# Kernel optimization log

Measured on AMD Instinct MI355X. Metric: run time of the kernel, lower is better.

The kernel has to match this reference:

```python
import jax, jax.numpy as jnp
import numpy as np

N, B, C, H = 1024, 4, 1024, 8
D = C // H  # head dim = 128


def setup_inputs() -> dict:
    key = jax.random.key(0)
    ks = jax.random.split(key, 10)
    f = lambda k, s: jax.random.normal(k, s, dtype=jnp.float32)
    w = lambda k: f(k, (C, C)) * 0.02  # torch Linear weight layout (out, in)
    return {
        "query_reg": f(ks[0], (N, B, C)),
        "key_reg": f(ks[1], (N, B, C)),
        "query_cls": f(ks[2], (N, B, C)),
        "key_cls": f(ks[3], (N, B, C)),
        "value": f(ks[4], (N, B, C)),
        "W_q_reg": w(ks[5]),
        "W_k_reg": w(ks[6]),
        "W_q_cls": w(ks[7]),
        "W_k_cls": w(ks[8]),
        "W_v": w(ks[9]),
    }


def _proj_heads(x, W):
    # x: (N, B, C); torch Linear: y = x @ W.T -> reshape (N,B,H,D) -> (B,H,N,D)
    y = jnp.einsum('nbc,dc->nbd', x, W)
    return y.reshape(N, B, H, D).transpose(1, 2, 0, 3)


def _l2norm(x):
    return x / jnp.linalg.norm(x, axis=-1, keepdims=True)


def reference(query_reg, key_reg, query_cls, key_cls, value,
              W_q_reg, W_k_reg, W_q_cls, W_k_cls, W_v):
    q_reg = _l2norm(_proj_heads(query_reg, W_q_reg))  # (B,H,N,D)
    k_reg = _l2norm(_proj_heads(key_reg, W_k_reg))
    q_cls = _l2norm(_proj_heads(query_cls, W_q_cls))
    k_cls = _l2norm(_proj_heads(key_cls, W_k_cls))
    v = _proj_heads(value, W_v)

    attn_reg = jax.nn.softmax(jnp.einsum('bhnd,bhmd->bhnm', q_reg, k_reg), axis=-1)
    attn_cls = jax.nn.softmax(jnp.einsum('bhnd,bhmd->bhnm', q_cls, k_cls), axis=-1)
    attn = (attn_reg + attn_cls) * 0.5  # (B,H,N,N)

    x = jnp.einsum('bhnm,bhmd->bhnd', attn, v)  # (B,H,N,D)
    x = x.transpose(0, 2, 1, 3).reshape(B, N, C)  # (B,N,C)
    return (x.transpose(1, 0, 2), attn)  # ((N,B,C), (B,H,N,N))
```

## Files before the change

kernel.cpp:

```cpp
#include <hip/hip_runtime.h>

#define DEVINL __device__ __forceinline__

typedef unsigned short u16;
typedef float f32x4 __attribute__((ext_vector_type(4)));
typedef __bf16 bf16x8 __attribute__((ext_vector_type(8)));

constexpr int N_ = 1024, B_ = 4, C_ = 1024, H_ = 8, D_ = 128;
constexpr int NB = N_ * B_;
constexpr int BH = B_ * H_;

DEVINL u16 f2bf(float f) {
  unsigned u = __builtin_bit_cast(unsigned, f);
  u += 0x7fffu + ((u >> 16) & 1u);
  return (u16)(u >> 16);
}
DEVINL float bf2f(u16 v) { return __builtin_bit_cast(float, ((unsigned)v) << 16); }

typedef __attribute__((address_space(1))) void gv_t;
typedef __attribute__((address_space(3))) void lv_t;
DEVINL void gload16(const void* g, void* l) {
  __builtin_amdgcn_global_load_lds((gv_t*)(unsigned long long)g,
                                   (lv_t*)(unsigned)(unsigned long long)l, 16, 0, 0);
}
DEVINL bf16x8 ld_frag(const u16* p) { return *(const bf16x8*)p; }
DEVINL f32x4 mfma16(bf16x8 a, bf16x8 b, f32x4 c) {
  return __builtin_amdgcn_mfma_f32_16x16x32_bf16(a, b, c, 0, 0, 0);
}

struct ConvArgs { const float* s[10]; u16* d[10]; int n[10]; };

__global__ __launch_bounds__(256) void k_convert(ConvArgs a) {
  const int which = blockIdx.y;
  const int i = (blockIdx.x * 256 + threadIdx.x) * 8;
  if (i >= a.n[which]) return;
  const float* s = a.s[which] + i;
  float4 v0 = *(const float4*)s;
  float4 v1 = *(const float4*)(s + 4);
  union { uint4 v; u16 r[8]; } u;
  u.r[0] = f2bf(v0.x); u.r[1] = f2bf(v0.y); u.r[2] = f2bf(v0.z); u.r[3] = f2bf(v0.w);
  u.r[4] = f2bf(v1.x); u.r[5] = f2bf(v1.y); u.r[6] = f2bf(v1.z); u.r[7] = f2bf(v1.w);
  *(uint4*)(a.d[which] + i) = u.v;
}

struct ProjArgs { const u16* X[5]; const u16* W[5]; u16* O[5]; };

__global__ __launch_bounds__(256) void k_proj(ProjArgs a) {
  __shared__ u16 lA[128 * 64];
  __shared__ u16 lB[128 * 64];
  __shared__ float lred[128][2];
  const int tid = threadIdx.x, w = tid >> 6, lane = tid & 63;
  const int qd = lane >> 4, m16 = lane & 15;
  const int wr = w >> 1, wc = w & 1;
  const int r0 = blockIdx.y * 128, d0 = blockIdx.x * 128;
  const u16* __restrict__ X = a.X[blockIdx.z];
  const u16* __restrict__ W = a.W[blockIdx.z];
  u16* __restrict__ O = a.O[blockIdx.z];
  const bool donorm = blockIdx.z < 4;

  f32x4 acc[4][4];
  const f32x4 fz = {0.f, 0.f, 0.f, 0.f};
#pragma unroll
  for (int i = 0; i < 4; ++i)
#pragma unroll
    for (int j = 0; j < 4; ++j) acc[i][j] = fz;

  for (int k0 = 0; k0 < C_; k0 += 64) {
    __syncthreads();
#pragma unroll
    for (int i = 0; i < 4; ++i) {
      int p = i * 256 + tid, row = p >> 3, cp = p & 7, cl = cp ^ (row & 7);
      gload16(X + (size_t)(r0 + row) * C_ + k0 + cl * 8, &lA[p * 8]);
    }
#pragma unroll
    for (int i = 0; i < 4; ++i) {
      int p = i * 256 + tid, row = p >> 3, cp = p & 7, cl = cp ^ (row & 7);
      gload16(W + (size_t)(d0 + row) * C_ + k0 + cl * 8, &lB[p * 8]);
    }
    __syncthreads();
#pragma unroll
    for (int ks = 0; ks < 2; ++ks) {
      bf16x8 af[4], bfr[4];
#pragma unroll
      for (int t = 0; t < 4; ++t) {
        int row = wr * 64 + t * 16 + m16;
        af[t] = ld_frag(&lA[row * 64 + (((ks * 4 + qd) ^ (row & 7)) * 8)]);
        int col = wc * 64 + t * 16 + m16;
        bfr[t] = ld_frag(&lB[col * 64 + (((ks * 4 + qd) ^ (col & 7)) * 8)]);
      }
#pragma unroll
      for (int rt = 0; rt < 4; ++rt)
#pragma unroll
        for (int ct = 0; ct < 4; ++ct)
          acc[rt][ct] = mfma16(af[rt], bfr[ct], acc[rt][ct]);
    }
  }
  if (donorm) {
    float s[4][4];
#pragma unroll
    for (int rt = 0; rt < 4; ++rt)
#pragma unroll
      for (int rg = 0; rg < 4; ++rg) {
        float t = 0.f;
#pragma unroll
        for (int ct = 0; ct < 4; ++ct) t += acc[rt][ct][rg] * acc[rt][ct][rg];
        s[rt][rg] = t;
      }
#pragma unroll
    for (int off = 1; off < 16; off <<= 1)
#pragma unroll
      for (int rt = 0; rt < 4; ++rt)
#pragma unroll
        for (int rg = 0; rg < 4; ++rg) s[rt][rg] += __shfl_xor(s[rt][rg], off);
    if (m16 == 0) {
#pragma unroll
      for (int rt = 0; rt < 4; ++rt)
#pragma unroll
        for (int rg = 0; rg < 4; ++rg)
          lred[wr * 64 + rt * 16 + qd * 4 + rg][wc] = s[rt][rg];
    }
  }
  __syncthreads();
  float inv[4][4];
#pragma unroll
  for (int rt = 0; rt < 4; ++rt)
#pragma unroll
    for (int rg = 0; rg < 4; ++rg) {
      if (donorm) {
        int row = wr * 64 + rt * 16 + qd * 4 + rg;
        inv[rt][rg] = rsqrtf(lred[row][0] + lred[row][1]);
      } else inv[rt][rg] = 1.0f;
    }
#pragma unroll
  for (int rt = 0; rt < 4; ++rt)
#pragma unroll
    for (int ct = 0; ct < 4; ++ct)
#pragma unroll
      for (int rg = 0; rg < 4; ++rg) {
        int row = r0 + wr * 64 + rt * 16 + qd * 4 + rg;
        int col = d0 + wc * 64 + ct * 16 + m16;
        int n = row >> 2, b = row & 3, h = col >> 7, d = col & 127;
        O[(((size_t)(b * H_ + h)) * N_ + n) * D_ + d] = f2bf(acc[rt][ct][rg] * inv[rt][rg]);
      }
}

__global__ __launch_bounds__(256) void k_transpose(const u16* __restrict__ v,
                                                   u16* __restrict__ vt) {
  __shared__ u16 tile[128][65];
  const int bh = blockIdx.y, n0 = blockIdx.x * 64;
  const u16* src = v + (size_t)bh * N_ * D_;
  u16* dst = vt + (size_t)bh * D_ * N_;
  union U8 { uint4 v; u16 s[8]; };
#pragma unroll
  for (int it = 0; it < 4; ++it) {
    int c = it * 256 + threadIdx.x;
    int n = c >> 4, dc = (c & 15) * 8;
    U8 u; u.v = *(const uint4*)(src + (size_t)(n0 + n) * D_ + dc);
#pragma unroll
    for (int j = 0; j < 8; ++j) tile[dc + j][n] = u.s[j];
  }
  __syncthreads();
#pragma unroll
  for (int it = 0; it < 4; ++it) {
    int c = it * 256 + threadIdx.x;
    int d = c >> 3, nc = (c & 7) * 8;
    U8 u;
#pragma unroll
    for (int j = 0; j < 8; ++j) u.s[j] = tile[d][nc + j];
    *(uint4*)(dst + (size_t)d * N_ + n0 + nc) = u.v;
  }
}

__global__ __launch_bounds__(512, 2) void k_attn(const u16* __restrict__ qr,
                                                 const u16* __restrict__ kr,
                                                 const u16* __restrict__ qc,
                                                 const u16* __restrict__ kc,
                                                 const u16* __restrict__ vt,
                                                 float* __restrict__ out0,
                                                 float* __restrict__ out1) {
  __shared__ u16 lP[2][32 * 136];
  __shared__ float lred[2][8][32];
  const int flat = blockIdx.x + (blockIdx.y << 5);
  const int xcd = flat & 7, kk = flat >> 3;
  const int bh = (xcd << 2) + (kk >> 5);
  const int n0 = (kk & 31) * 32;
  const int b = bh >> 3, h = bh & 7;
  const size_t base = (size_t)bh * N_ * D_;
  const int tid = threadIdx.x, w = tid >> 6, lane = tid & 63;
  const int qd = lane >> 4, m16 = lane & 15;

  bf16x8 qf[2][2][4];
#pragma unroll
  for (int ct = 0; ct < 2; ++ct)
#pragma unroll
    for (int ks = 0; ks < 4; ++ks) {
      size_t ro = base + (size_t)(n0 + ct * 16 + m16) * D_ + ks * 32 + qd * 8;
      qf[0][ct][ks] = ld_frag(qr + ro);
      qf[1][ct][ks] = ld_frag(qc + ro);
    }

  const u16* krp = kr + base + (size_t)(w * 16 + m16) * D_;
  const u16* kcp = kc + base + (size_t)(w * 16 + m16) * D_;

  uint2 pst[2][8][2];
  float psum[2][2] = {{0.f, 0.f}, {0.f, 0.f}};
  const f32x4 fz = {0.f, 0.f, 0.f, 0.f};

#pragma unroll
  for (int mt = 0; mt < 8; ++mt) {
    const size_t moff = (size_t)mt * 128 * D_;
#pragma unroll
    for (int ty = 0; ty < 2; ++ty) {
      const u16* kp = (ty ? kcp : krp) + moff;
      bf16x8 af[4];
#pragma unroll
      for (int ks = 0; ks < 4; ++ks)
        af[ks] = ld_frag(kp + ks * 32 + qd * 8);
#pragma unroll
      for (int ct = 0; ct < 2; ++ct) {
        f32x4 acc = fz;
#pragma unroll
        for (int ks = 0; ks < 4; ++ks) acc = mfma16(af[ks], qf[ty][ct][ks], acc);
        union { uint2 u; u16 s[4]; } pk;
        float loc = 0.f;
#pragma unroll
        for (int rg = 0; rg < 4; ++rg) {
          float e = __expf(acc[rg]);
          loc += e;
          pk.s[rg] = f2bf(e);
        }
        psum[ty][ct] += loc;
        pst[ty][mt][ct] = pk.u;
      }
    }
  }

#pragma unroll
  for (int ty = 0; ty < 2; ++ty)
#pragma unroll
    for (int ct = 0; ct < 2; ++ct) {
      psum[ty][ct] += __shfl_xor(psum[ty][ct], 16);
      psum[ty][ct] += __shfl_xor(psum[ty][ct], 32);
    }
  if (qd == 0) {
#pragma unroll
    for (int ty = 0; ty < 2; ++ty)
#pragma unroll
      for (int ct = 0; ct < 2; ++ct) lred[ty][w][ct * 16 + m16] = psum[ty][ct];
  }
  __syncthreads();
  float il[2][2];
#pragma unroll
  for (int ty = 0; ty < 2; ++ty)
#pragma unroll
    for (int ct = 0; ct < 2; ++ct) {
      int n = ct * 16 + m16;
      float s = 0.f;
#pragma unroll
      for (int ww = 0; ww < 8; ++ww) s += lred[ty][ww][n];
      il[ty][ct] = 0.5f / s;
    }

  f32x4 xacc[2] = {fz, fz};
  float* attn = out1 + (size_t)bh * N_ * N_;
  const u16* vtb = vt + (size_t)bh * D_ * N_ + (size_t)(w * 16 + m16) * N_;

#pragma unroll
  for (int mt = 0; mt < 8; ++mt) {
    const int cur = mt & 1;
    const int m0 = mt * 128;
#pragma unroll
    for (int ct = 0; ct < 2; ++ct) {
      union { uint2 u; u16 s[4]; } ur, uc, pk;
      ur.u = pst[0][mt][ct];
      uc.u = pst[1][mt][ct];
      f32x4 pv;
#pragma unroll
      for (int rg = 0; rg < 4; ++rg) {
        pv[rg] = bf2f(ur.s[rg]) * il[0][ct] + bf2f(uc.s[rg]) * il[1][ct];
        pk.s[rg] = f2bf(pv[rg]);
      }
      const int nrow = n0 + ct * 16 + m16;
      const int mcol = m0 + w * 16 + qd * 4;
      *(f32x4*)(attn + (size_t)nrow * N_ + mcol) = pv;
      *(uint2*)&lP[cur][(ct * 16 + m16) * 136 + w * 16 + qd * 4] = pk.u;
    }
    __syncthreads();
#pragma unroll
    for (int ks = 0; ks < 4; ++ks) {
      bf16x8 pa[2];
#pragma unroll
      for (int ct = 0; ct < 2; ++ct)
        pa[ct] = ld_frag(&lP[cur][(ct * 16 + m16) * 136 + ks * 32 + qd * 8]);
      bf16x8 vb = ld_frag(vtb + m0 + ks * 32 + qd * 8);
#pragma unroll
      for (int ct = 0; ct < 2; ++ct)
        xacc[ct] = mfma16(pa[ct], vb, xacc[ct]);
    }
  }
#pragma unroll
  for (int ct = 0; ct < 2; ++ct)
#pragma unroll
    for (int rg = 0; rg < 4; ++rg) {
      int n = n0 + ct * 16 + qd * 4 + rg;
      int d = w * 16 + m16;
      out0[((size_t)n * B_ + b) * C_ + h * 128 + d] = xacc[ct][rg];
    }
}

extern "C" void kernel_launch(void* const* d_in, const int* in_sizes, int n_in,
                              void* d_out, int out_size, void* d_ws, size_t ws_size,
                              hipStream_t stream) {
  (void)in_sizes; (void)n_in; (void)out_size; (void)ws_size;
  const float* in_f[10];
  for (int i = 0; i < 10; ++i) in_f[i] = (const float*)d_in[i];

  u16* ws = (u16*)d_ws;
  u16* Xc[5], *Wc[5], *P[5];
  for (int i = 0; i < 5; ++i) Xc[i] = ws + (size_t)i * NB * C_;
  u16* wbase = ws + (size_t)5 * NB * C_;
  for (int i = 0; i < 5; ++i) Wc[i] = wbase + (size_t)i * C_ * C_;
  u16* pbase = wbase + (size_t)5 * C_ * C_;
  for (int i = 0; i < 5; ++i) P[i] = pbase + (size_t)i * BH * N_ * D_;
  u16* vt = pbase + (size_t)5 * BH * N_ * D_;

  float* out0 = (float*)d_out;
  float* out1 = out0 + (size_t)N_ * B_ * C_;

  ConvArgs ca;
  for (int i = 0; i < 5; ++i) { ca.s[i] = in_f[i];     ca.d[i] = Xc[i];  ca.n[i] = NB * C_; }
  for (int i = 0; i < 5; ++i) { ca.s[5+i] = in_f[5+i]; ca.d[5+i] = Wc[i]; ca.n[5+i] = C_ * C_; }
  k_convert<<<dim3(2048, 10), 256, 0, stream>>>(ca);

  ProjArgs pa;
  for (int i = 0; i < 5; ++i) { pa.X[i] = Xc[i]; pa.W[i] = Wc[i]; pa.O[i] = P[i]; }
  k_proj<<<dim3(C_ / 128, NB / 128, 5), 256, 0, stream>>>(pa);

  k_transpose<<<dim3(N_ / 64, BH), 256, 0, stream>>>(P[4], vt);

  k_attn<<<dim3(N_ / 32, BH), 512, 0, stream>>>(P[0], P[1], P[2], P[3], vt, out0, out1);
}
```

Measured before the change: 422.5 us.

## Stage K tiles in LDS for attention and swizzle projection block order

The attention kernel now copies each 128-row K tile for both branches into swizzled LDS buffers using global_load_lds, and all waves read their MFMA fragments from LDS instead of each wave loading them from global memory. The P buffer becomes single-buffered, with extra barriers to keep reuse safe. The launch bound is raised to ask for 4 blocks per CU, and the projection kernel remaps its block index for XCD-friendly ordering. The trade-off is a larger LDS footprint plus extra syncs per tile, and a much tighter register budget that may cause spills of the large pst array.

```diff
diff --git a/kernel.cpp b/kernel.cpp
--- a/kernel.cpp
+++ b/kernel.cpp
@@ -52,11 +52,14 @@
   const int tid = threadIdx.x, w = tid >> 6, lane = tid & 63;
   const int qd = lane >> 4, m16 = lane & 15;
   const int wr = w >> 1, wc = w & 1;
-  const int r0 = blockIdx.y * 128, d0 = blockIdx.x * 128;
-  const u16* __restrict__ X = a.X[blockIdx.z];
-  const u16* __restrict__ W = a.W[blockIdx.z];
-  u16* __restrict__ O = a.O[blockIdx.z];
-  const bool donorm = blockIdx.z < 4;
+  const int flat = blockIdx.x + (blockIdx.y << 3) + (blockIdx.z << 8);
+  const int swz = (flat & 7) * 160 + (flat >> 3);
+  const int bz = swz >> 8, rem = swz & 255, by = rem >> 3, bx = rem & 7;
+  const int r0 = by * 128, d0 = bx * 128;
+  const u16* __restrict__ X = a.X[bz];
+  const u16* __restrict__ W = a.W[bz];
+  u16* __restrict__ O = a.O[bz];
+  const bool donorm = bz < 4;
 
   f32x4 acc[4][4];
   const f32x4 fz = {0.f, 0.f, 0.f, 0.f};
@@ -171,14 +174,15 @@
   }
 }
 
-__global__ __launch_bounds__(512, 2) void k_attn(const u16* __restrict__ qr,
+__global__ __launch_bounds__(512, 4) void k_attn(const u16* __restrict__ qr,
                                                  const u16* __restrict__ kr,
                                                  const u16* __restrict__ qc,
                                                  const u16* __restrict__ kc,
                                                  const u16* __restrict__ vt,
                                                  float* __restrict__ out0,
                                                  float* __restrict__ out1) {
-  __shared__ u16 lP[2][32 * 136];
+  __shared__ u16 lK[2][128 * 128];
+  __shared__ u16 lP[32 * 136];
   __shared__ float lred[2][8][32];
   const int flat = blockIdx.x + (blockIdx.y << 5);
   const int xcd = flat & 7, kk = flat >> 3;
@@ -188,6 +192,7 @@
   const size_t base = (size_t)bh * N_ * D_;
   const int tid = threadIdx.x, w = tid >> 6, lane = tid & 63;
   const int qd = lane >> 4, m16 = lane & 15;
+  const u16* ksrc[2] = {kr, kc};
 
   bf16x8 qf[2][2][4];
 #pragma unroll
@@ -199,23 +204,29 @@
       qf[1][ct][ks] = ld_frag(qc + ro);
     }
 
-  const u16* krp = kr + base + (size_t)(w * 16 + m16) * D_;
-  const u16* kcp = kc + base + (size_t)(w * 16 + m16) * D_;
-
   uint2 pst[2][8][2];
   float psum[2][2] = {{0.f, 0.f}, {0.f, 0.f}};
   const f32x4 fz = {0.f, 0.f, 0.f, 0.f};
 
 #pragma unroll
   for (int mt = 0; mt < 8; ++mt) {
-    const size_t moff = (size_t)mt * 128 * D_;
+    const int m0 = mt * 128;
+    __syncthreads();
+#pragma unroll
+    for (int ty = 0; ty < 2; ++ty)
+#pragma unroll
+      for (int i = 0; i < 4; ++i) {
+        int p = i * 512 + tid, row = p >> 4, cp = p & 15, cl = cp ^ (row & 15);
+        gload16(ksrc[ty] + base + (size_t)(m0 + row) * D_ + cl * 8, &lK[ty][p * 8]);
+      }
+    __syncthreads();
+    const int mrow = w * 16 + m16;
 #pragma unroll
     for (int ty = 0; ty < 2; ++ty) {
-      const u16* kp = (ty ? kcp : krp) + moff;
       bf16x8 af[4];
 #pragma unroll
       for (int ks = 0; ks < 4; ++ks)
-        af[ks] = ld_frag(kp + ks * 32 + qd * 8);
+        af[ks] = ld_frag(&lK[ty][mrow * 128 + (((ks * 4 + qd) ^ (mrow & 15)) * 8)]);
 #pragma unroll
       for (int ct = 0; ct < 2; ++ct) {
         f32x4 acc = fz;
@@ -242,6 +253,7 @@
       psum[ty][ct] += __shfl_xor(psum[ty][ct], 16);
       psum[ty][ct] += __shfl_xor(psum[ty][ct], 32);
     }
+  __syncthreads();
   if (qd == 0) {
 #pragma unroll
     for (int ty = 0; ty < 2; ++ty)
@@ -267,7 +279,6 @@
 
 #pragma unroll
   for (int mt = 0; mt < 8; ++mt) {
-    const int cur = mt & 1;
     const int m0 = mt * 128;
 #pragma unroll
     for (int ct = 0; ct < 2; ++ct) {
@@ -283,7 +294,7 @@
       const int nrow = n0 + ct * 16 + m16;
       const int mcol = m0 + w * 16 + qd * 4;
       *(f32x4*)(attn + (size_t)nrow * N_ + mcol) = pv;
-      *(uint2*)&lP[cur][(ct * 16 + m16) * 136 + w * 16 + qd * 4] = pk.u;
+      *(uint2*)&lP[(ct * 16 + m16) * 136 + w * 16 + qd * 4] = pk.u;
     }
     __syncthreads();
 #pragma unroll
@@ -291,12 +302,13 @@
       bf16x8 pa[2];
 #pragma unroll
       for (int ct = 0; ct < 2; ++ct)
-        pa[ct] = ld_frag(&lP[cur][(ct * 16 + m16) * 136 + ks * 32 + qd * 8]);
+        pa[ct] = ld_frag(&lP[(ct * 16 + m16) * 136 + ks * 32 + qd * 8]);
       bf16x8 vb = ld_frag(vtb + m0 + ks * 32 + qd * 8);
 #pragma unroll
       for (int ct = 0; ct < 2; ++ct)
         xacc[ct] = mfma16(pa[ct], vb, xacc[ct]);
     }
+    __syncthreads();
   }
 #pragma unroll
   for (int ct = 0; ct < 2; ++ct)
```

After: 443.1 us. +4.9%, slower.
